# Optimization experiments

Measured on AMD Instinct MI355X. Metric: run time of the kernel, lower is better.

The kernel has to match this reference:

```python
import jax, jax.numpy as jnp
import numpy as np

DIM = 768
HEADS = 12
DIM_HEAD = 64
INNER = HEADS * DIM_HEAD  # 768
EPS = 1e-5


def setup_inputs() -> dict:
    key = jax.random.key(0)
    ks = jax.random.split(key, 5)
    x = jax.random.normal(ks[0], (4, 2048, DIM), dtype=jnp.float32)
    ln_g = jnp.ones((DIM,), dtype=jnp.float32)
    ln_b = jnp.zeros((DIM,), dtype=jnp.float32)
    s1 = 1.0 / np.sqrt(DIM)
    W_qkv = jax.random.uniform(ks[1], (DIM, 3 * INNER), dtype=jnp.float32, minval=-s1, maxval=s1)
    b_qkv = jax.random.uniform(ks[2], (3 * INNER,), dtype=jnp.float32, minval=-s1, maxval=s1)
    s2 = 1.0 / np.sqrt(INNER)
    W_out = jax.random.uniform(ks[3], (INNER, DIM), dtype=jnp.float32, minval=-s2, maxval=s2)
    b_out = jax.random.uniform(ks[4], (DIM,), dtype=jnp.float32, minval=-s2, maxval=s2)
    return {"x": x, "ln_g": ln_g, "ln_b": ln_b, "W_qkv": W_qkv, "b_qkv": b_qkv, "W_out": W_out, "b_out": b_out}


def reference(x, ln_g, ln_b, W_qkv, b_qkv, W_out, b_out):
    b, n, _ = x.shape
    # pre-norm LayerNorm
    mu = jnp.mean(x, axis=-1, keepdims=True)
    var = jnp.mean(jnp.square(x - mu), axis=-1, keepdims=True)
    xn = (x - mu) * jax.lax.rsqrt(var + EPS) * ln_g + ln_b
    qkv = xn @ W_qkv + b_qkv  # [b, n, 3*inner]
    q, k, v = jnp.split(qkv, 3, axis=-1)
    def to_heads(t):
        return t.reshape(b, n, HEADS, DIM_HEAD).transpose(0, 2, 1, 3)  # b h n d
    q, k, v = map(to_heads, (q, k, v))
    q = q * (DIM_HEAD ** -0.5)
    sim = jnp.einsum('bhid,bhjd->bhij', q, k)
    attn = jax.nn.softmax(sim, axis=-1)  # dropout is identity (p=0.0)
    out = jnp.einsum('bhij,bhjd->bhid', attn, v)
    out = out.transpose(0, 2, 1, 3).reshape(b, n, INNER)
    return out @ W_out + b_out
```

## Files before the change

### kernel.cpp

```cpp
#include <hip/hip_runtime.h>
#include <cstdint>
#include <cstddef>


#define SEQ    2048
#define NBATCH 4
#define DMODEL 768
#define NHEADS 12
#define DHEAD  64
#define MROWS  (NBATCH * SEQ)
#define NQKV   (3 * DMODEL)
#define KT     64
#define NT     (SEQ / KT)

using f32x4  = __attribute__((ext_vector_type(4))) float;
using u16x8  = __attribute__((ext_vector_type(8))) unsigned short;
using s16x8  = __attribute__((ext_vector_type(8))) short;
using u16x4  = __attribute__((ext_vector_type(4))) unsigned short;
using s16x4  = __attribute__((ext_vector_type(4))) short;

__device__ __forceinline__ unsigned short f2bf(float f) {
  union { float f; unsigned int u; } x; x.f = f;
  unsigned int r = x.u + 0x7fffu + ((x.u >> 16) & 1u);
  return (unsigned short)(r >> 16);
}

#if defined(__has_builtin)
#if __has_builtin(__builtin_amdgcn_cvt_pk_bf16_f32)
#define HAVE_PK_BF16 1
#endif
#if __has_builtin(__builtin_amdgcn_exp2f)
#define HAVE_EXP2 1
#endif
#if __has_builtin(__builtin_amdgcn_mfma_f32_16x16x16bf16_1k)
#define HAVE_MFMA_16X16X16_BF16 1
#endif
#endif

__device__ __forceinline__ unsigned int pk_bf16(float a, float b) {
#ifdef HAVE_PK_BF16
  auto v = __builtin_amdgcn_cvt_pk_bf16_f32(a, b);
  union { decltype(v) v2; unsigned int u; } c; c.v2 = v; return c.u;
#else
  return (unsigned int)f2bf(a) | ((unsigned int)f2bf(b) << 16);
#endif
}

__device__ __forceinline__ float fexp2(float x) {
#ifdef HAVE_EXP2
  return __builtin_amdgcn_exp2f(x);
#else
  return exp2f(x);
#endif
}

__device__ __forceinline__ f32x4 mfma16(u16x8 a, u16x8 b, f32x4 c) {
  return __builtin_amdgcn_mfma_f32_16x16x32_bf16((s16x8)a, (s16x8)b, c, 0, 0, 0);
}

__device__ __forceinline__ f32x4 mfma16k16(u16x4 a, u16x4 b, f32x4 c) {
#ifdef HAVE_MFMA_16X16X16_BF16
  return __builtin_amdgcn_mfma_f32_16x16x16bf16_1k((s16x4)a, (s16x4)b, c, 0, 0, 0);
#else
  f32x4 d;
  asm("v_mfma_f32_16x16x16_bf16 %0, %1, %2, %3"
      : "=v"(d) : "v"(a), "v"(b), "v"(c));
  return d;
#endif
}

__device__ __forceinline__ void gl_lds16(const void* g, void* l) {
  __builtin_amdgcn_global_load_lds(
      (const __attribute__((address_space(1))) void*)g,
      (__attribute__((address_space(3))) void*)l, 16, 0, 0);
}

__global__ __launch_bounds__(256) void ln_kernel(
    const float* __restrict__ x, const float* __restrict__ g,
    const float* __restrict__ bb, unsigned short* __restrict__ xn) {
  __shared__ float red[8];
  const int row = blockIdx.x, t = threadIdx.x;
  const float* xr = x + (size_t)row * DMODEL;
  float v0 = xr[t], v1 = xr[t + 256], v2 = xr[t + 512];
  float s = v0 + v1 + v2;
#pragma unroll
  for (int o = 32; o; o >>= 1) s += __shfl_down(s, o);
  if ((t & 63) == 0) red[t >> 6] = s;
  __syncthreads();
  float mu = (red[0] + red[1] + red[2] + red[3]) * (1.0f / DMODEL);
  float d0 = v0 - mu, d1 = v1 - mu, d2 = v2 - mu;
  float q = d0 * d0 + d1 * d1 + d2 * d2;
#pragma unroll
  for (int o = 32; o; o >>= 1) q += __shfl_down(q, o);
  if ((t & 63) == 0) red[4 + (t >> 6)] = q;
  __syncthreads();
  float var = (red[4] + red[5] + red[6] + red[7]) * (1.0f / DMODEL);
  float rstd = rsqrtf(var + 1e-5f);
  size_t base = (size_t)row * DMODEL;
  xn[base + t]       = f2bf(d0 * rstd * g[t]       + bb[t]);
  xn[base + t + 256] = f2bf(d1 * rstd * g[t + 256] + bb[t + 256]);
  xn[base + t + 512] = f2bf(d2 * rstd * g[t + 512] + bb[t + 512]);
}

__global__ __launch_bounds__(256) void tconv2_kernel(
    const float* __restrict__ Wq, const float* __restrict__ Wo,
    unsigned short* __restrict__ Wqt, unsigned short* __restrict__ Wot) {
  __shared__ float tile[32][33];
  int id = blockIdx.x;
  const float* W; unsigned short* Wt; int N, n0, k0;
  if (id < 1728) { W = Wq; Wt = Wqt; N = NQKV;   n0 = (id % 72) * 32; k0 = (id / 72) * 32; }
  else { id -= 1728; W = Wo; Wt = Wot; N = DMODEL; n0 = (id % 24) * 32; k0 = (id / 24) * 32; }
  const int tx = threadIdx.x & 31, ty = threadIdx.x >> 5;
#pragma unroll
  for (int r = 0; r < 4; ++r)
    tile[ty + r * 8][tx] = W[(size_t)(k0 + ty + r * 8) * N + n0 + tx];
  __syncthreads();
#pragma unroll
  for (int r = 0; r < 4; ++r)
    Wt[(size_t)(n0 + ty + r * 8) * DMODEL + k0 + tx] = f2bf(tile[tx][ty + r * 8]);
}

__global__ __launch_bounds__(256, 3) void gemm_qkv_kernel(
    const unsigned short* __restrict__ Wt, const unsigned short* __restrict__ xn,
    const float* __restrict__ bias, unsigned short* __restrict__ qb,
    unsigned short* __restrict__ kb, unsigned short* __restrict__ vt) {
  __shared__ alignas(16) unsigned short As[128 * 64];
  __shared__ alignas(16) unsigned short Bs[128 * 64];
  const int t = threadIdx.x, wid = t >> 6, l = t & 63, quad = l >> 4, ll = l & 15;
  const int bid = blockIdx.x;
  const int w = (bid & 7) * 144 + (bid >> 3);
  const bool isqk = (w < 768);
  int a0, b0;
  if (isqk) { a0 = (w % 12) * 128; b0 = (w / 12) * 128; }
  else { int w2 = w - 768; a0 = (w2 & 63) * 128; b0 = 2 * DMODEL + (w2 >> 6) * 128; }
  const unsigned short* Ap = isqk ? (Wt + (size_t)a0 * DMODEL) : (xn + (size_t)a0 * DMODEL);
  const unsigned short* Bp = isqk ? (xn + (size_t)b0 * DMODEL) : (Wt + (size_t)b0 * DMODEL);
  const int wa = (wid >> 1) * 64, wb = (wid & 1) * 64;
  const int srow = l >> 3, sblk = (l & 7) ^ srow;
  f32x4 acc[4][4] = {};
  for (int k0 = 0; k0 < DMODEL; k0 += 64) {
#pragma unroll
    for (int cc = 0; cc < 4; ++cc) {
      int call = wid * 4 + cc;
      int r = call * 8 + srow;
      gl_lds16(Ap + (size_t)r * DMODEL + k0 + sblk * 8, &As[call * 512]);
      gl_lds16(Bp + (size_t)r * DMODEL + k0 + sblk * 8, &Bs[call * 512]);
    }
    __syncthreads();
#pragma unroll
    for (int ks = 0; ks < 2; ++ks) {
      u16x8 af[4], bf[4];
#pragma unroll
      for (int i = 0; i < 4; ++i) {
        int ra = wa + i * 16 + ll, rb = wb + i * 16 + ll;
        int blk = (ks * 4 + quad) ^ (ll & 7);
        af[i] = *(const u16x8*)&As[ra * 64 + blk * 8];
        bf[i] = *(const u16x8*)&Bs[rb * 64 + blk * 8];
      }
#pragma unroll
      for (int mi = 0; mi < 4; ++mi)
#pragma unroll
        for (int ni = 0; ni < 4; ++ni)
          acc[mi][ni] = mfma16(af[mi], bf[ni], acc[mi][ni]);
    }
    __syncthreads();
  }
  if (isqk) {
    const bool isq = (a0 < DMODEL);
    unsigned short* dst = isq ? qb : kb;
    const float sc = isq ? 0.18033688f : 1.0f;
#pragma unroll
    for (int mi = 0; mi < 4; ++mi) {
      int row0 = a0 + wa + mi * 16 + quad * 4;
      float4 bv = *(const float4*)&bias[row0];
      int rr = isq ? row0 : row0 - DMODEL;
      int h = rr >> 6, d0 = rr & 63;
#pragma unroll
      for (int ni = 0; ni < 4; ++ni) {
        int seq = b0 + wb + ni * 16 + ll;
        int b = seq >> 11, i = seq & 2047;
        uint2 pk;
        pk.x = pk_bf16((acc[mi][ni][0] + bv.x) * sc, (acc[mi][ni][1] + bv.y) * sc);
        pk.y = pk_bf16((acc[mi][ni][2] + bv.z) * sc, (acc[mi][ni][3] + bv.w) * sc);
        *(uint2*)&dst[(size_t)((b * NHEADS + h) * SEQ + i) * DHEAD + d0] = pk;
      }
    }
  } else {
#pragma unroll
    for (int mi = 0; mi < 4; ++mi) {
      int gm = a0 + wa + mi * 16 + quad * 4;
      int b = gm >> 11, i0 = gm & 2047;
#pragma unroll
      for (int ni = 0; ni < 4; ++ni) {
        int gn = b0 + wb + ni * 16 + ll;
        float bv = bias[gn];
        int rem = gn - 2 * DMODEL;
        int h = rem >> 6, d = rem & 63;
        int bh = b * NHEADS + h;
        uint2 pk;
        pk.x = pk_bf16(acc[mi][ni][0] + bv, acc[mi][ni][1] + bv);
        pk.y = pk_bf16(acc[mi][ni][2] + bv, acc[mi][ni][3] + bv);
        *(uint2*)&vt[((size_t)bh * DHEAD + d) * SEQ + i0] = pk;
      }
    }
  }
}

__global__ __launch_bounds__(256, 3) void attn_kernel(
    const unsigned short* __restrict__ qbuf, const unsigned short* __restrict__ kbuf,
    const unsigned short* __restrict__ vtg, unsigned short* __restrict__ ao) {
  __shared__ alignas(16) unsigned short stage[3][2][KT * DHEAD];
  const int t = threadIdx.x, wid = t >> 6, l = t & 63, quad = l >> 4, ll = l & 15;
  const int Lid = blockIdx.y * 16 + blockIdx.x;
  const int w = (Lid & 7) * 96 + (Lid >> 3);
  const int qt = w & 15, bh = w >> 4;
  const unsigned short* qg  = qbuf + ((size_t)bh * SEQ + qt * 128) * DHEAD;
  const unsigned short* kg0 = kbuf + (size_t)bh * SEQ * DHEAD;
  const unsigned short* vt0 = vtg  + (size_t)bh * DHEAD * SEQ;
  const int srow = l >> 3;
  const int sblk = (l & 7) ^ srow;

  unsigned short* Qs = &stage[0][0][0];
#pragma unroll
  for (int cc = 0; cc < 4; ++cc) {
    int call = wid * 4 + cc;
    gl_lds16(qg + (call * 8 + srow) * 64 + sblk * 8, Qs + call * 512);
  }
  __syncthreads();
  u16x8 qf[2][2];
#pragma unroll
  for (int mi = 0; mi < 2; ++mi)
#pragma unroll
    for (int ks = 0; ks < 2; ++ks) {
      int r = wid * 32 + mi * 16 + ll;
      int blk = (ks * 4 + quad) ^ (ll & 7);
      qf[mi][ks] = *(const u16x8*)&Qs[r * 64 + blk * 8];
    }
  __syncthreads();

  auto stage_tile = [&](int buf, int kt2) {
    const unsigned short* kg = kg0 + (size_t)kt2 * KT * DHEAD;
#pragma unroll
    for (int c = 0; c < 2; ++c) {
      int call = wid * 2 + c;
      int r = call * 8 + srow;
      gl_lds16(kg + r * 64 + sblk * 8, &stage[buf][0][call * 512]);
      gl_lds16(vt0 + (size_t)r * SEQ + kt2 * KT + sblk * 8, &stage[buf][1][call * 512]);
    }
  };

  f32x4 oacc[2][4] = {};
  f32x4 osum[2] = {};
  const u16x4 onesb = {0x3f80u, 0x3f80u, 0x3f80u, 0x3f80u};

  stage_tile(0, 0);
  stage_tile(1, 1);
  int bufc = 0, bufs = 2;
  for (int kt2 = 0; kt2 < NT; ++kt2) {
    if (kt2 + 1 < NT) asm volatile("s_waitcnt vmcnt(4)" ::: "memory");
    else              asm volatile("s_waitcnt vmcnt(0)" ::: "memory");
    __builtin_amdgcn_s_barrier();
    if (kt2 + 2 < NT) stage_tile(bufs, kt2 + 2);
    const unsigned short* Ks = &stage[bufc][0][0];
    const unsigned short* Vs = &stage[bufc][1][0];

    f32x4 st[2][4] = {};
    __builtin_amdgcn_s_setprio(1);
#pragma unroll
    for (int ks = 0; ks < 2; ++ks)
#pragma unroll
      for (int ni = 0; ni < 4; ++ni) {
        int r = ni * 16 + ll;
        int blk = (ks * 4 + quad) ^ (ll & 7);
        u16x8 kf = *(const u16x8*)&Ks[r * 64 + blk * 8];
        st[0][ni] = mfma16(kf, qf[0][ks], st[0][ni]);
        st[1][ni] = mfma16(kf, qf[1][ks], st[1][ni]);
      }
    __builtin_amdgcn_s_setprio(0);

#pragma unroll
    for (int ni = 0; ni < 4; ++ni) {
      u16x4 pf[2];
#pragma unroll
      for (int mi = 0; mi < 2; ++mi) {
        float p0 = fexp2(st[mi][ni][0]);
        float p1 = fexp2(st[mi][ni][1]);
        float p2 = fexp2(st[mi][ni][2]);
        float p3 = fexp2(st[mi][ni][3]);
        union { uint2 u; u16x4 v; } cv;
        cv.u.x = pk_bf16(p0, p1);
        cv.u.y = pk_bf16(p2, p3);
        pf[mi] = cv.v;
      }
      const int voff = (((ni * 2 + (quad >> 1)) ^ (ll & 7)) << 3) + (quad & 1) * 4;
      __builtin_amdgcn_s_setprio(1);
      osum[0] = mfma16k16(pf[0], onesb, osum[0]);
      osum[1] = mfma16k16(pf[1], onesb, osum[1]);
#pragma unroll
      for (int di = 0; di < 4; ++di) {
        u16x4 vf = *(const u16x4*)&Vs[(di * 16 + ll) * 64 + voff];
        oacc[0][di] = mfma16k16(pf[0], vf, oacc[0][di]);
        oacc[1][di] = mfma16k16(pf[1], vf, oacc[1][di]);
      }
      __builtin_amdgcn_s_setprio(0);
    }
    bufc = (bufc == 2) ? 0 : bufc + 1;
    bufs = (bufs == 2) ? 0 : bufs + 1;
  }

  const int b = bh / NHEADS, h = bh - b * NHEADS;
#pragma unroll
  for (int mi = 0; mi < 2; ++mi) {
#pragma unroll
    for (int r = 0; r < 4; ++r) {
      float inv = 1.0f / osum[mi][r];
      int row = qt * 128 + wid * 32 + mi * 16 + quad * 4 + r;
      size_t base = ((size_t)(b * SEQ + row)) * DMODEL + h * DHEAD;
#pragma unroll
      for (int di = 0; di < 4; ++di)
        ao[base + di * 16 + ll] = f2bf(oacc[mi][di][r] * inv);
    }
  }
}

__global__ __launch_bounds__(256, 3) void gemm_out_kernel(
    const unsigned short* __restrict__ Wt, const unsigned short* __restrict__ ao,
    const float* __restrict__ bias, float* __restrict__ out) {
  __shared__ alignas(16) unsigned short As[64 * 64];
  __shared__ alignas(16) unsigned short Bs[128 * 64];
  const int t = threadIdx.x, wid = t >> 6, l = t & 63, quad = l >> 4, ll = l & 15;
  const int a0 = blockIdx.x * 64;
  const int b0 = blockIdx.y * 128;
  const int wa = (wid >> 1) * 32, wb = (wid & 1) * 64;
  const int srow = l >> 3, sblk = (l & 7) ^ srow;
  f32x4 acc[2][4] = {};
  for (int k0 = 0; k0 < DMODEL; k0 += 64) {
#pragma unroll
    for (int cc = 0; cc < 6; ++cc) {
      int call = wid * 6 + cc;
      if (call < 8) {
        int r = call * 8 + srow;
        gl_lds16(Wt + (size_t)(a0 + r) * DMODEL + k0 + sblk * 8, &As[call * 512]);
      } else {
        int c2 = call - 8;
        int r = c2 * 8 + srow;
        gl_lds16(ao + (size_t)(b0 + r) * DMODEL + k0 + sblk * 8, &Bs[c2 * 512]);
      }
    }
    __syncthreads();
#pragma unroll
    for (int ks = 0; ks < 2; ++ks) {
      u16x8 af[2], bf[4];
#pragma unroll
      for (int i = 0; i < 2; ++i) {
        int ra = wa + i * 16 + ll;
        int blk = (ks * 4 + quad) ^ (ll & 7);
        af[i] = *(const u16x8*)&As[ra * 64 + blk * 8];
      }
#pragma unroll
      for (int i = 0; i < 4; ++i) {
        int rb = wb + i * 16 + ll;
        int blk = (ks * 4 + quad) ^ (ll & 7);
        bf[i] = *(const u16x8*)&Bs[rb * 64 + blk * 8];
      }
#pragma unroll
      for (int mi = 0; mi < 2; ++mi)
#pragma unroll
        for (int ni = 0; ni < 4; ++ni)
          acc[mi][ni] = mfma16(af[mi], bf[ni], acc[mi][ni]);
    }
    __syncthreads();
  }
#pragma unroll
  for (int mi = 0; mi < 2; ++mi) {
    int row0 = a0 + wa + mi * 16 + quad * 4;
    float4 bv = *(const float4*)&bias[row0];
#pragma unroll
    for (int ni = 0; ni < 4; ++ni) {
      int seq = b0 + wb + ni * 16 + ll;
      float4 o;
      o.x = acc[mi][ni][0] + bv.x;
      o.y = acc[mi][ni][1] + bv.y;
      o.z = acc[mi][ni][2] + bv.z;
      o.w = acc[mi][ni][3] + bv.w;
      *(float4*)&out[(size_t)seq * DMODEL + row0] = o;
    }
  }
}

extern "C" void kernel_launch(void* const* d_in, const int* in_sizes, int n_in,
                              void* d_out, int out_size, void* d_ws, size_t ws_size,
                              hipStream_t stream) {
  const float* x     = (const float*)d_in[0];
  const float* ln_g  = (const float*)d_in[1];
  const float* ln_b  = (const float*)d_in[2];
  const float* W_qkv = (const float*)d_in[3];
  const float* b_qkv = (const float*)d_in[4];
  const float* W_out = (const float*)d_in[5];
  const float* b_out = (const float*)d_in[6];
  float* out = (float*)d_out;

  char* ws = (char*)d_ws;
  unsigned short* xn    = (unsigned short*)(ws);
  unsigned short* wqkvt = (unsigned short*)(ws + 12582912);
  unsigned short* woutt = (unsigned short*)(ws + 16121856);
  unsigned short* qb    = (unsigned short*)(ws + 17301504);
  unsigned short* kb    = (unsigned short*)(ws + 29884416);
  unsigned short* vt    = (unsigned short*)(ws + 42467328);
  unsigned short* ao    = xn;

  ln_kernel<<<MROWS, 256, 0, stream>>>(x, ln_g, ln_b, xn);
  tconv2_kernel<<<2304, 256, 0, stream>>>(W_qkv, W_out, wqkvt, woutt);
  gemm_qkv_kernel<<<1152, 256, 0, stream>>>(wqkvt, xn, b_qkv, qb, kb, vt);
  attn_kernel<<<dim3(SEQ / 128, NBATCH * NHEADS), 256, 0, stream>>>(qb, kb, vt, ao);
  gemm_out_kernel<<<dim3(12, 64), 256, 0, stream>>>(woutt, ao, b_out, out);
}
```

Baseline: 226.1 us.

## Load K/V fragments directly from global memory instead of LDS staging in attention

```diff
diff --git a/kernel.cpp b/kernel.cpp
--- a/kernel.cpp
+++ b/kernel.cpp
@@ -209,7 +209,7 @@
 __global__ __launch_bounds__(256, 3) void attn_kernel(
     const unsigned short* __restrict__ qbuf, const unsigned short* __restrict__ kbuf,
     const unsigned short* __restrict__ vtg, unsigned short* __restrict__ ao) {
-  __shared__ alignas(16) unsigned short stage[3][2][KT * DHEAD];
+  __shared__ alignas(16) unsigned short Qs[128 * 64];
   const int t = threadIdx.x, wid = t >> 6, l = t & 63, quad = l >> 4, ll = l & 15;
   const int Lid = blockIdx.y * 16 + blockIdx.x;
   const int w = (Lid & 7) * 96 + (Lid >> 3);
@@ -220,7 +220,6 @@
   const int srow = l >> 3;
   const int sblk = (l & 7) ^ srow;
 
-  unsigned short* Qs = &stage[0][0][0];
 #pragma unroll
   for (int cc = 0; cc < 4; ++cc) {
     int call = wid * 4 + cc;
@@ -236,33 +235,25 @@
       int blk = (ks * 4 + quad) ^ (ll & 7);
       qf[mi][ks] = *(const u16x8*)&Qs[r * 64 + blk * 8];
     }
-  __syncthreads();
-
-  auto stage_tile = [&](int buf, int kt2) {
-    const unsigned short* kg = kg0 + (size_t)kt2 * KT * DHEAD;
-#pragma unroll
-    for (int c = 0; c < 2; ++c) {
-      int call = wid * 2 + c;
-      int r = call * 8 + srow;
-      gl_lds16(kg + r * 64 + sblk * 8, &stage[buf][0][call * 512]);
-      gl_lds16(vt0 + (size_t)r * SEQ + kt2 * KT + sblk * 8, &stage[buf][1][call * 512]);
-    }
-  };
 
   f32x4 oacc[2][4] = {};
   f32x4 osum[2] = {};
   const u16x4 onesb = {0x3f80u, 0x3f80u, 0x3f80u, 0x3f80u};
 
-  stage_tile(0, 0);
-  stage_tile(1, 1);
-  int bufc = 0, bufs = 2;
+  const unsigned short* kbase = kg0 + ll * 64;
+  const unsigned short* vbase = vt0 + (size_t)ll * SEQ + quad * 4;
+
+#pragma unroll 1
   for (int kt2 = 0; kt2 < NT; ++kt2) {
-    if (kt2 + 1 < NT) asm volatile("s_waitcnt vmcnt(4)" ::: "memory");
-    else              asm volatile("s_waitcnt vmcnt(0)" ::: "memory");
-    __builtin_amdgcn_s_barrier();
-    if (kt2 + 2 < NT) stage_tile(bufs, kt2 + 2);
-    const unsigned short* Ks = &stage[bufc][0][0];
-    const unsigned short* Vs = &stage[bufc][1][0];
+    const unsigned short* kp = kbase + kt2 * (KT * DHEAD);
+    const unsigned short* vp = vbase + kt2 * KT;
+
+    u16x8 kf[2][4];
+#pragma unroll
+    for (int ks = 0; ks < 2; ++ks)
+#pragma unroll
+      for (int ni = 0; ni < 4; ++ni)
+        kf[ks][ni] = *(const u16x8*)&kp[ni * (16 * 64) + (ks * 4 + quad) * 8];
 
     f32x4 st[2][4] = {};
     __builtin_amdgcn_s_setprio(1);
@@ -270,13 +261,17 @@
     for (int ks = 0; ks < 2; ++ks)
 #pragma unroll
       for (int ni = 0; ni < 4; ++ni) {
-        int r = ni * 16 + ll;
-        int blk = (ks * 4 + quad) ^ (ll & 7);
-        u16x8 kf = *(const u16x8*)&Ks[r * 64 + blk * 8];
-        st[0][ni] = mfma16(kf, qf[0][ks], st[0][ni]);
-        st[1][ni] = mfma16(kf, qf[1][ks], st[1][ni]);
+        st[0][ni] = mfma16(kf[ks][ni], qf[0][ks], st[0][ni]);
+        st[1][ni] = mfma16(kf[ks][ni], qf[1][ks], st[1][ni]);
       }
     __builtin_amdgcn_s_setprio(0);
+
+    u16x4 vf[4][4];
+#pragma unroll
+    for (int ni = 0; ni < 4; ++ni)
+#pragma unroll
+      for (int di = 0; di < 4; ++di)
+        vf[ni][di] = *(const u16x4*)&vp[(size_t)di * (16 * SEQ) + ni * 16];
 
 #pragma unroll
     for (int ni = 0; ni < 4; ++ni) {
@@ -292,20 +287,16 @@
         cv.u.y = pk_bf16(p2, p3);
         pf[mi] = cv.v;
       }
-      const int voff = (((ni * 2 + (quad >> 1)) ^ (ll & 7)) << 3) + (quad & 1) * 4;
       __builtin_amdgcn_s_setprio(1);
       osum[0] = mfma16k16(pf[0], onesb, osum[0]);
       osum[1] = mfma16k16(pf[1], onesb, osum[1]);
 #pragma unroll
       for (int di = 0; di < 4; ++di) {
-        u16x4 vf = *(const u16x4*)&Vs[(di * 16 + ll) * 64 + voff];
-        oacc[0][di] = mfma16k16(pf[0], vf, oacc[0][di]);
-        oacc[1][di] = mfma16k16(pf[1], vf, oacc[1][di]);
+        oacc[0][di] = mfma16k16(pf[0], vf[ni][di], oacc[0][di]);
+        oacc[1][di] = mfma16k16(pf[1], vf[ni][di], oacc[1][di]);
       }
       __builtin_amdgcn_s_setprio(0);
     }
-    bufc = (bufc == 2) ? 0 : bufc + 1;
-    bufs = (bufs == 2) ? 0 : bufs + 1;
   }
 
   const int b = bh / NHEADS, h = bh - b * NHEADS;
```

Result: slower. 423.4 us (+87.2%).

## Software-pipeline attention loop: overlap previous tile's PV MFMAs with current exp

Applied to the files above, without the earlier changes.

```diff
diff --git a/kernel.cpp b/kernel.cpp
--- a/kernel.cpp
+++ b/kernel.cpp
@@ -252,19 +252,10 @@
   f32x4 oacc[2][4] = {};
   f32x4 osum[2] = {};
   const u16x4 onesb = {0x3f80u, 0x3f80u, 0x3f80u, 0x3f80u};
-
-  stage_tile(0, 0);
-  stage_tile(1, 1);
-  int bufc = 0, bufs = 2;
-  for (int kt2 = 0; kt2 < NT; ++kt2) {
-    if (kt2 + 1 < NT) asm volatile("s_waitcnt vmcnt(4)" ::: "memory");
-    else              asm volatile("s_waitcnt vmcnt(0)" ::: "memory");
-    __builtin_amdgcn_s_barrier();
-    if (kt2 + 2 < NT) stage_tile(bufs, kt2 + 2);
-    const unsigned short* Ks = &stage[bufc][0][0];
-    const unsigned short* Vs = &stage[bufc][1][0];
-
-    f32x4 st[2][4] = {};
+  u16x4 pf[2][4];
+  u16x4 vfr[4][4];
+
+  auto qk_cluster = [&](const unsigned short* Ks, f32x4 st[2][4]) {
     __builtin_amdgcn_s_setprio(1);
 #pragma unroll
     for (int ks = 0; ks < 2; ++ks)
@@ -277,36 +268,76 @@
         st[1][ni] = mfma16(kf, qf[1][ks], st[1][ni]);
       }
     __builtin_amdgcn_s_setprio(0);
-
+  };
+  auto pv_ni = [&](int ni) {
+    osum[0] = mfma16k16(pf[0][ni], onesb, osum[0]);
+    osum[1] = mfma16k16(pf[1][ni], onesb, osum[1]);
+#pragma unroll
+    for (int di = 0; di < 4; ++di) {
+      oacc[0][di] = mfma16k16(pf[0][ni], vfr[ni][di], oacc[0][di]);
+      oacc[1][di] = mfma16k16(pf[1][ni], vfr[ni][di], oacc[1][di]);
+    }
+  };
+  auto exp_ni = [&](f32x4 st[2][4], int ni) {
+#pragma unroll
+    for (int mi = 0; mi < 2; ++mi) {
+      float p0 = fexp2(st[mi][ni][0]);
+      float p1 = fexp2(st[mi][ni][1]);
+      float p2 = fexp2(st[mi][ni][2]);
+      float p3 = fexp2(st[mi][ni][3]);
+      union { uint2 u; u16x4 v; } cv;
+      cv.u.x = pk_bf16(p0, p1);
+      cv.u.y = pk_bf16(p2, p3);
+      pf[mi][ni] = cv.v;
+    }
+  };
+  auto loadv = [&](const unsigned short* Vs) {
 #pragma unroll
     for (int ni = 0; ni < 4; ++ni) {
-      u16x4 pf[2];
-#pragma unroll
-      for (int mi = 0; mi < 2; ++mi) {
-        float p0 = fexp2(st[mi][ni][0]);
-        float p1 = fexp2(st[mi][ni][1]);
-        float p2 = fexp2(st[mi][ni][2]);
-        float p3 = fexp2(st[mi][ni][3]);
-        union { uint2 u; u16x4 v; } cv;
-        cv.u.x = pk_bf16(p0, p1);
-        cv.u.y = pk_bf16(p2, p3);
-        pf[mi] = cv.v;
-      }
       const int voff = (((ni * 2 + (quad >> 1)) ^ (ll & 7)) << 3) + (quad & 1) * 4;
-      __builtin_amdgcn_s_setprio(1);
-      osum[0] = mfma16k16(pf[0], onesb, osum[0]);
-      osum[1] = mfma16k16(pf[1], onesb, osum[1]);
-#pragma unroll
-      for (int di = 0; di < 4; ++di) {
-        u16x4 vf = *(const u16x4*)&Vs[(di * 16 + ll) * 64 + voff];
-        oacc[0][di] = mfma16k16(pf[0], vf, oacc[0][di]);
-        oacc[1][di] = mfma16k16(pf[1], vf, oacc[1][di]);
-      }
-      __builtin_amdgcn_s_setprio(0);
-    }
+#pragma unroll
+      for (int di = 0; di < 4; ++di)
+        vfr[ni][di] = *(const u16x4*)&Vs[(di * 16 + ll) * 64 + voff];
+    }
+  };
+
+  stage_tile(0, 0);
+  stage_tile(1, 1);
+
+  asm volatile("s_waitcnt vmcnt(4)" ::: "memory");
+  __builtin_amdgcn_s_barrier();
+  stage_tile(2, 2);
+  {
+    f32x4 st[2][4] = {};
+    qk_cluster(&stage[0][0][0], st);
+#pragma unroll
+    for (int ni = 0; ni < 4; ++ni) exp_ni(st, ni);
+    loadv(&stage[0][1][0]);
+  }
+
+  int bufc = 1, bufs = 0;
+#pragma unroll 1
+  for (int kt2 = 1; kt2 < NT; ++kt2) {
+    if (kt2 + 1 < NT) asm volatile("s_waitcnt vmcnt(4) lgkmcnt(0)" ::: "memory");
+    else              asm volatile("s_waitcnt vmcnt(0) lgkmcnt(0)" ::: "memory");
+    __builtin_amdgcn_s_barrier();
+    if (kt2 + 2 < NT) stage_tile(bufs, kt2 + 2);
+    const unsigned short* Ks = &stage[bufc][0][0];
+    const unsigned short* Vs = &stage[bufc][1][0];
+
+    f32x4 st[2][4] = {};
+    qk_cluster(Ks, st);
+#pragma unroll
+    for (int ni = 0; ni < 4; ++ni) {
+      pv_ni(ni);
+      exp_ni(st, ni);
+    }
+    loadv(Vs);
     bufc = (bufc == 2) ? 0 : bufc + 1;
     bufs = (bufs == 2) ? 0 : bufs + 1;
   }
+#pragma unroll
+  for (int ni = 0; ni < 4; ++ni) pv_ni(ni);
 
   const int b = bh / NHEADS, h = bh - b * NHEADS;
 #pragma unroll
```

Result: slower. 247.9 us (+9.6%).
